# Kernel tuning notes

Measured on AMD Instinct MI355X. Metric: run time of the kernel, lower is better.

The kernel has to match this reference:

```python
import math
import jax, jax.numpy as jnp
import numpy as np

B, T, C, H = 2, 2048, 1024, 16
MAX_SEQ = 2048


def _make_pe(max_seq: int, dim: int, base: float = 10000.0) -> np.ndarray:
    pe = np.zeros((max_seq, dim), dtype=np.float32)
    position = np.arange(max_seq, dtype=np.float32)[:, None]
    div_term = np.exp(np.arange(0, dim, 2, dtype=np.float32) * (-math.log(base) / dim))
    pe[:, 0::2] = np.sin(position * div_term)
    pe[:, 1::2] = np.cos(position * div_term)
    return pe


def setup_inputs() -> dict:
    key = jax.random.key(0)
    k1, k2, k3 = jax.random.split(key, 3)
    x = jax.random.normal(k1, (B, T, C), dtype=jnp.float32)
    # torch Linear default init scale ~ 1/sqrt(fan_in)
    w_qkv = jax.random.normal(k2, (3 * C, C), dtype=jnp.float32) / math.sqrt(C)
    w_proj = jax.random.normal(k3, (C, C), dtype=jnp.float32) / math.sqrt(C)
    pe = jnp.asarray(_make_pe(MAX_SEQ, C))
    return {"x": x, "w_qkv": w_qkv, "w_proj": w_proj, "pe": pe}


def reference(x, w_qkv, w_proj, pe):
    b, t, c = x.shape
    h = H
    d = c // h
    # RoPE module adds sinusoidal PE under torch.no_grad() -> stop_gradient
    xp = jax.lax.stop_gradient(x + pe[None, :t, :])
    qkv = xp @ w_qkv.T  # [b, t, 3c]
    q, k, v = jnp.split(qkv, 3, axis=-1)
    q = q.reshape(b, t, h, d).transpose(0, 2, 1, 3)  # bhtd
    k = k.reshape(b, t, h, d).transpose(0, 2, 1, 3)
    v = v.reshape(b, t, h, d).transpose(0, 2, 1, 3)
    att = jnp.einsum("bhqd,bhkd->bhqk", q, k) * (1.0 / math.sqrt(d))
    causal = jnp.tril(jnp.ones((t, t), dtype=bool))  # [t, t]
    att = jnp.where(causal[None, None], att, -jnp.inf)
    att = jax.nn.softmax(att, axis=-1)
    y = jnp.einsum("bhqk,bhkd->bhqd", att, v)
    y = y.transpose(0, 2, 1, 3).reshape(b, t, c)
    return y @ w_proj.T
```

## Files before the change

kernel.cpp:

```cpp
#include <hip/hip_runtime.h>
#include <cstdint>

typedef __bf16 bf16x8 __attribute__((ext_vector_type(8)));
typedef __bf16 bf16x4 __attribute__((ext_vector_type(4)));
typedef float  f32x4  __attribute__((ext_vector_type(4)));

static constexpr int kB = 2, kT = 2048, kC = 1024, kH = 16, kD = 64;
static constexpr int kK = 1024;

__device__ __forceinline__ uint16_t f2bf(float f) {
  uint32_t u = __builtin_bit_cast(uint32_t, f);
  u += 0x7FFFu + ((u >> 16) & 1u);
  return (uint16_t)(u >> 16);
}

__device__ __forceinline__ void gl_lds16(const void* g, void* l) {
  __builtin_amdgcn_global_load_lds((__attribute__((address_space(1))) void*)(void*)g,
                                   (__attribute__((address_space(3))) void*)l, 16, 0, 0);
}

__global__ __launch_bounds__(256) void prep_all(const float* __restrict__ x,
                                                const float* __restrict__ pe,
                                                const float* __restrict__ wqkv,
                                                const float* __restrict__ wproj,
                                                uint16_t* __restrict__ xp,
                                                uint16_t* __restrict__ wq,
                                                uint16_t* __restrict__ wp) {
  constexpr int NX = kB * kT * kC / 4;
  constexpr int NWQ = 3 * kC * kC / 4;
  const int i = blockIdx.x * 256 + threadIdx.x;
  if (i < NX) {
    const float4 xv = ((const float4*)x)[i];
    const int c4 = i & (kC / 4 - 1);
    const int t = (i / (kC / 4)) & (kT - 1);
    const float4 pv = ((const float4*)pe)[t * (kC / 4) + c4];
    ushort4 o;
    o.x = f2bf(xv.x + pv.x);
    o.y = f2bf(xv.y + pv.y);
    o.z = f2bf(xv.z + pv.z);
    o.w = f2bf(xv.w + pv.w);
    ((ushort4*)xp)[i] = o;
  } else if (i < NX + NWQ) {
    const int j = i - NX;
    const float4 v = ((const float4*)wqkv)[j];
    ushort4 u;
    u.x = f2bf(v.x); u.y = f2bf(v.y); u.z = f2bf(v.z); u.w = f2bf(v.w);
    ((ushort4*)wq)[j] = u;
  } else {
    const int j = i - NX - NWQ;
    const float4 v = ((const float4*)wproj)[j];
    ushort4 u;
    u.x = f2bf(v.x); u.y = f2bf(v.y); u.z = f2bf(v.z); u.w = f2bf(v.w);
    ((ushort4*)wp)[j] = u;
  }
}

__global__ __launch_bounds__(512, 2) void gemm_qkv(const uint16_t* __restrict__ A,
                                                   const uint16_t* __restrict__ W,
                                                   uint16_t* __restrict__ qb,
                                                   uint16_t* __restrict__ kb,
                                                   uint16_t* __restrict__ vT) {
  __shared__ __align__(1024) char lds[114688];
  const int tid = threadIdx.x;
  const int lane = tid & 63;
  const int wid = tid >> 6;
  const int l15 = lane & 15, l4 = lane >> 4;
  const int WM = wid >> 2, WN = wid & 3;
  const int orig = (int)blockIdx.x;
  const int xcd = orig & 7, j = orig >> 3;
  const int m0 = (xcd * 2 + (j & 1)) * 256;
  const int n0 = (j >> 1) * 192;

  f32x4 acc[2][4][3] = {};
  bf16x8 bfp[2][3];

  auto stageA = [&](int buf, int kt) {
#pragma unroll
    for (int c = 0; c < 4; ++c) {
      const int off = (c * 512 + tid) * 16;
      const int lr = off >> 7, cbl = off & 127;
      gl_lds16((const char*)A + ((size_t)(m0 + lr) * kK + kt * 64) * 2 +
                   (cbl ^ ((lr & 7) << 4)),
               lds + buf * 32768 + off);
    }
  };
  auto stageB = [&](int buf, int kt) {
#pragma unroll
    for (int c = 0; c < 3; ++c) {
      const int off = (c * 512 + tid) * 16;
      const int lr = off >> 7, cbl = off & 127;
      gl_lds16((const char*)W + ((size_t)(n0 + lr) * kK + kt * 64) * 2 +
                   (cbl ^ ((lr & 7) << 4)),
               lds + 65536 + buf * 24576 + off);
    }
  };

#define QKV_PHASE(CBUF, H, SA, SBUF, KT, VM)                                      \
  {                                                                               \
    if (SA) stageA(SBUF, KT); else stageB(SBUF, KT);                              \
    if (VM == 4)                                                                  \
      asm volatile("s_waitcnt vmcnt(4)" ::: "memory");                            \
    else                                                                          \
      asm volatile("s_waitcnt vmcnt(7)" ::: "memory");                            \
    __builtin_amdgcn_s_barrier();                                                 \
    asm volatile("" ::: "memory");                                                \
    const char* Ab = lds + (CBUF)*32768;                                          \
    const char* Bb = lds + 65536 + (CBUF)*24576;                                  \
    if ((H) == 0) {                                                               \
      _Pragma("unroll") for (int ks = 0; ks < 2; ++ks)                            \
          _Pragma("unroll") for (int nt = 0; nt < 3; ++nt) {                      \
        const int lr = WN * 48 + nt * 16 + l15;                                   \
        bfp[ks][nt] = *(const bf16x8*)(Bb + lr * 128 +                            \
                                       ((ks * 64 + l4 * 16) ^ ((lr & 7) << 4)));  \
      }                                                                           \
    }                                                                             \
    _Pragma("unroll") for (int ks = 0; ks < 2; ++ks) {                            \
      bf16x8 af[4];                                                               \
      _Pragma("unroll") for (int mt = 0; mt < 4; ++mt) {                          \
        const int lr = (H)*128 + WM * 64 + mt * 16 + l15;                         \
        af[mt] = *(const bf16x8*)(Ab + lr * 128 +                                 \
                                  ((ks * 64 + l4 * 16) ^ ((lr & 7) << 4)));       \
      }                                                                           \
      __builtin_amdgcn_s_setprio(1);                                              \
      _Pragma("unroll") for (int mt = 0; mt < 4; ++mt)                            \
          _Pragma("unroll") for (int nt = 0; nt < 3; ++nt)                        \
              acc[H][mt][nt] = __builtin_amdgcn_mfma_f32_16x16x32_bf16(           \
                  af[mt], bfp[ks][nt], acc[H][mt][nt], 0, 0, 0);                  \
      __builtin_amdgcn_s_setprio(0);                                              \
    }                                                                             \
    asm volatile("" ::: "memory");                                                \
    __builtin_amdgcn_s_barrier();                                                 \
    asm volatile("" ::: "memory");                                                \
  }

  stageA(0, 0);
  stageB(0, 0);

  for (int i = 0; i < 8; ++i) {
    const int ktb1 = 2 * i + 1;
    const int ktb0 = (2 * i + 2 > 15) ? 15 : 2 * i + 2;
    QKV_PHASE(0, 0, 1, 1, ktb1, 4);
    QKV_PHASE(0, 1, 0, 1, ktb1, 7);
    QKV_PHASE(1, 0, 1, 0, ktb0, 4);
    QKV_PHASE(1, 1, 0, 0, ktb0, 7);
  }
  asm volatile("s_waitcnt vmcnt(0)" ::: "memory");
  __builtin_amdgcn_s_barrier();
  asm volatile("" ::: "memory");

  const int b = m0 >> 11, tb = m0 & (kT - 1);
#pragma unroll
  for (int h = 0; h < 2; ++h)
#pragma unroll
    for (int mt = 0; mt < 4; ++mt)
#pragma unroll
      for (int nt = 0; nt < 3; ++nt)
#pragma unroll
        for (int r = 0; r < 4; ++r) {
          const int m = h * 128 + WM * 64 + mt * 16 + l4 * 4 + r;
          const int t = tb + m;
          const int n = n0 + WN * 48 + nt * 16 + l15;
          const int sec = n >> 10, nn = n & (kC - 1);
          const int hh = nn >> 6, d = nn & 63;
          const uint16_t v = f2bf(acc[h][mt][nt][r]);
          if (sec == 0)
            qb[((size_t)((b * kH + hh) * kT + t)) * kD + d] = v;
          else if (sec == 1)
            kb[((size_t)((b * kH + hh) * kT + t)) * kD + d] = v;
          else
            vT[((size_t)((b * kH + hh) * kD + d)) * kT + t] = v;
        }
#undef QKV_PHASE
}

__global__ __launch_bounds__(256, 2) void gemm_proj(const uint16_t* __restrict__ A,
                                                    const uint16_t* __restrict__ W,
                                                    float* __restrict__ out) {
  __shared__ __align__(1024) char lds[65536];
  const int tid = threadIdx.x;
  const int lane = tid & 63;
  const int wid = tid >> 6;
  const int l15 = lane & 15, l4 = lane >> 4;
  const int WM = wid >> 1, WN = wid & 1;
  const int orig = (int)blockIdx.x;
  const int xcd = orig & 7, j = orig >> 3;
  const int m0 = (xcd * 4 + (j & 3)) * 128;
  const int n0 = (j >> 2) * 128;

  f32x4 acc[2][2][4] = {};
  bf16x8 bfp[2][4];

  auto stage = [&](int isA, int buf, int kt) {
#pragma unroll
    for (int c = 0; c < 4; ++c) {
      const int off = (c * 256 + tid) * 16;
      const int lr = off >> 7, cbl = off & 127;
      const size_t grow = (size_t)((isA ? m0 : n0) + lr) * kK + kt * 64;
      gl_lds16((const char*)(isA ? A : W) + grow * 2 + (cbl ^ ((lr & 7) << 4)),
               lds + (isA ? 0 : 32768) + buf * 16384 + off);
    }
  };

#define PRJ_PHASE(CBUF, H, SA, SBUF, KT, VM)                                      \
  {                                                                               \
    stage(SA, SBUF, KT);                                                          \
    if (VM == 4)                                                                  \
      asm volatile("s_waitcnt vmcnt(4)" ::: "memory");                            \
    else                                                                          \
      asm volatile("s_waitcnt vmcnt(8)" ::: "memory");                            \
    __builtin_amdgcn_s_barrier();                                                 \
    asm volatile("" ::: "memory");                                                \
    const char* Ab = lds + (CBUF)*16384;                                          \
    const char* Bb = lds + 32768 + (CBUF)*16384;                                  \
    if ((H) == 0) {                                                               \
      _Pragma("unroll") for (int ks = 0; ks < 2; ++ks)                            \
          _Pragma("unroll") for (int nt = 0; nt < 4; ++nt) {                      \
        const int lr = WN * 64 + nt * 16 + l15;                                   \
        bfp[ks][nt] = *(const bf16x8*)(Bb + lr * 128 +                            \
                                       ((ks * 64 + l4 * 16) ^ ((lr & 7) << 4)));  \
      }                                                                           \
    }                                                                             \
    _Pragma("unroll") for (int ks = 0; ks < 2; ++ks) {                            \
      bf16x8 af[2];                                                               \
      _Pragma("unroll") for (int mt = 0; mt < 2; ++mt) {                          \
        const int lr = (H)*64 + WM * 32 + mt * 16 + l15;                          \
        af[mt] = *(const bf16x8*)(Ab + lr * 128 +                                 \
                                  ((ks * 64 + l4 * 16) ^ ((lr & 7) << 4)));       \
      }                                                                           \
      __builtin_amdgcn_s_setprio(1);                                              \
      _Pragma("unroll") for (int mt = 0; mt < 2; ++mt)                            \
          _Pragma("unroll") for (int nt = 0; nt < 4; ++nt)                        \
              acc[H][mt][nt] = __builtin_amdgcn_mfma_f32_16x16x32_bf16(           \
                  af[mt], bfp[ks][nt], acc[H][mt][nt], 0, 0, 0);                  \
      __builtin_amdgcn_s_setprio(0);                                              \
    }                                                                             \
    asm volatile("" ::: "memory");                                                \
    __builtin_amdgcn_s_barrier();                                                 \
    asm volatile("" ::: "memory");                                                \
  }

  stage(1, 0, 0);
  stage(0, 0, 0);

  for (int i = 0; i < 8; ++i) {
    const int ktb1 = 2 * i + 1;
    const int ktb0 = (2 * i + 2 > 15) ? 15 : 2 * i + 2;
    PRJ_PHASE(0, 0, 1, 1, ktb1, 4);
    PRJ_PHASE(0, 1, 0, 1, ktb1, 8);
    PRJ_PHASE(1, 0, 1, 0, ktb0, 4);
    PRJ_PHASE(1, 1, 0, 0, ktb0, 8);
  }
  asm volatile("s_waitcnt vmcnt(0)" ::: "memory");
  __builtin_amdgcn_s_barrier();
  asm volatile("" ::: "memory");

#pragma unroll
  for (int h = 0; h < 2; ++h)
#pragma unroll
    for (int mt = 0; mt < 2; ++mt)
#pragma unroll
      for (int nt = 0; nt < 4; ++nt)
#pragma unroll
        for (int r = 0; r < 4; ++r) {
          const int m = m0 + h * 64 + WM * 32 + mt * 16 + l4 * 4 + r;
          const int n = n0 + WN * 64 + nt * 16 + l15;
          out[(size_t)m * kC + n] = acc[h][mt][nt][r];
        }
#undef PRJ_PHASE
}

__global__ __launch_bounds__(256, 4) void attn(const uint16_t* __restrict__ qb,
                                               const uint16_t* __restrict__ kb,
                                               const uint16_t* __restrict__ vT,
                                               uint16_t* __restrict__ y) {
  __shared__ __align__(1024) char lds[40960];
  const int lane = threadIdx.x & 63;
  const int wid = threadIdx.x >> 6;
  const int l15 = lane & 15, l4 = lane >> 4;
  const int bh = blockIdx.x;
  const int qt = (int)(gridDim.y - 1) - (int)blockIdx.y;
  const int q0 = qt * 64 + wid * 16;
  const size_t base = (size_t)bh * kT * kD;
  const uint16_t* Q = qb + base;
  const uint16_t* Kp = kb + base;
  const uint16_t* Vt = vT + base;
  char* P = lds + 32768 + wid * 2048;
  const int xr = (l15 & 7) << 4;

  bf16x8 qf[2];
#pragma unroll
  for (int ks = 0; ks < 2; ++ks) {
    bf16x8 t = *(const bf16x8*)(Q + (size_t)(q0 + l15) * kD + ks * 32 + l4 * 8);
#pragma unroll
    for (int i = 0; i < 8; ++i) t[i] = (__bf16)((float)t[i] * 0.1803368801f);
    qf[ks] = t;
  }
  bf16x8 ones;
#pragma unroll
  for (int i = 0; i < 8; ++i) ones[i] = (__bf16)1.0f;

  float m_ = -1e30f;
  f32x4 o[4];
  f32x4 ol = {0.f, 0.f, 0.f, 0.f};
#pragma unroll
  for (int nt = 0; nt < 4; ++nt) o[nt] = (f32x4){0.f, 0.f, 0.f, 0.f};

  const int nkt = qt + 1;

  auto STAGE = [&](int bi, int k0) {
#pragma unroll
    for (int c = 0; c < 2; ++c) {
      const int call = wid * 2 + c;
      const int row = call * 8 + (lane >> 3);
      const int colb = (((lane & 7) ^ ((lane >> 3) & 7)) << 4);
      gl_lds16((const char*)Kp + ((size_t)(k0 + row) * kD) * 2 + colb,
               lds + bi * 8192 + call * 1024);
      gl_lds16((const char*)Vt + ((size_t)row * kT + k0) * 2 + colb,
               lds + 16384 + bi * 8192 + call * 1024);
    }
  };

  int cur = 0;
  STAGE(0, 0);
  for (int kt = 0; kt < nkt; ++kt) {
    const int k0 = kt * 64;
    const bool hasnext = (kt + 1 < nkt);
    if (hasnext) STAGE(cur ^ 1, k0 + 64);
    if (hasnext)
      asm volatile("s_waitcnt vmcnt(4)" ::: "memory");
    else
      asm volatile("s_waitcnt vmcnt(0)" ::: "memory");
    __builtin_amdgcn_s_barrier();
    asm volatile("" ::: "memory");

    const char* Kb = lds + cur * 8192;
    const char* Vb = lds + 16384 + cur * 8192;

    f32x4 s[4] = {};
    __builtin_amdgcn_s_setprio(1);
#pragma unroll
    for (int ks = 0; ks < 2; ++ks)
#pragma unroll
      for (int nt = 0; nt < 4; ++nt) {
        const bf16x8 kf =
            *(const bf16x8*)(Kb + (nt * 16 + l15) * 128 + ((ks * 64 + l4 * 16) ^ xr));
        s[nt] = __builtin_amdgcn_mfma_f32_16x16x32_bf16(kf, qf[ks], s[nt], 0, 0, 0);
      }
    __builtin_amdgcn_s_setprio(0);

    if (kt == nkt - 1) {
      const int qq = q0 + l15;
#pragma unroll
      for (int nt = 0; nt < 4; ++nt)
#pragma unroll
        for (int r = 0; r < 4; ++r)
          if (k0 + nt * 16 + l4 * 4 + r > qq) s[nt][r] = -1e30f;
    }

    float pm = s[0][0];
#pragma unroll
    for (int nt = 0; nt < 4; ++nt)
#pragma unroll
      for (int r = 0; r < 4; ++r) pm = fmaxf(pm, s[nt][r]);
    if (!__all(pm <= m_ + 11.0f)) {
      float rm = fmaxf(pm, __shfl_xor(pm, 16));
      rm = fmaxf(rm, __shfl_xor(rm, 32));
      const float newm = fmaxf(m_, rm);
      const float sc = exp2f(m_ - newm);
      m_ = newm;
#pragma unroll
      for (int nt = 0; nt < 4; ++nt)
#pragma unroll
        for (int r = 0; r < 4; ++r) o[nt][r] *= sc;
#pragma unroll
      for (int r = 0; r < 4; ++r) ol[r] *= sc;
    }
#pragma unroll
    for (int nt = 0; nt < 4; ++nt)
#pragma unroll
      for (int r = 0; r < 4; ++r) s[nt][r] = exp2f(s[nt][r] - m_);

#pragma unroll
    for (int nt = 0; nt < 4; ++nt) {
      bf16x4 pk;
#pragma unroll
      for (int r = 0; r < 4; ++r) pk[r] = (__bf16)s[nt][r];
      *(bf16x4*)(P + l15 * 128 + ((nt * 32 + l4 * 8) ^ xr)) = pk;
    }
    asm volatile("s_waitcnt lgkmcnt(0)" ::: "memory");
    __builtin_amdgcn_sched_barrier(0);

    bf16x8 pf[2];
#pragma unroll
    for (int ks = 0; ks < 2; ++ks)
      pf[ks] = *(const bf16x8*)(P + l15 * 128 + ((ks * 64 + l4 * 16) ^ xr));
    __builtin_amdgcn_s_setprio(1);
#pragma unroll
    for (int ks = 0; ks < 2; ++ks) {
#pragma unroll
      for (int nt = 0; nt < 4; ++nt) {
        const bf16x8 vf =
            *(const bf16x8*)(Vb + (nt * 16 + l15) * 128 + ((ks * 64 + l4 * 16) ^ xr));
        o[nt] = __builtin_amdgcn_mfma_f32_16x16x32_bf16(vf, pf[ks], o[nt], 0, 0, 0);
      }
      ol = __builtin_amdgcn_mfma_f32_16x16x32_bf16(ones, pf[ks], ol, 0, 0, 0);
    }
    __builtin_amdgcn_s_setprio(0);

    __builtin_amdgcn_s_barrier();
    asm volatile("" ::: "memory");
    cur ^= 1;
  }

  const float inv = 1.0f / ol[0];
  const int b = bh >> 4, h = bh & 15;
  const int q = q0 + l15;
#pragma unroll
  for (int nt = 0; nt < 4; ++nt) {
    bf16x4 yv;
#pragma unroll
    for (int r = 0; r < 4; ++r) yv[r] = (__bf16)(o[nt][r] * inv);
    *(bf16x4*)(y + ((size_t)(b * kT + q)) * kC + h * kD + nt * 16 + l4 * 4) = yv;
  }
}

extern "C" void kernel_launch(void* const* d_in, const int* in_sizes, int n_in,
                              void* d_out, int out_size, void* d_ws, size_t ws_size,
                              hipStream_t stream) {
  const float* x = (const float*)d_in[0];
  const float* wqkv = (const float*)d_in[1];
  const float* wproj = (const float*)d_in[2];
  const float* pe = (const float*)d_in[3];

  char* ws = (char*)d_ws;
  uint16_t* xp = (uint16_t*)(ws);
  uint16_t* wq = (uint16_t*)(ws + (size_t)(8u << 20));
  uint16_t* wp = (uint16_t*)(ws + (size_t)(14u << 20));
  uint16_t* qbuf = (uint16_t*)(ws + (size_t)(16u << 20));
  uint16_t* kbuf = (uint16_t*)(ws + (size_t)(24u << 20));
  uint16_t* vTb = (uint16_t*)(ws + (size_t)(32u << 20));

  prep_all<<<dim3(8192), 256, 0, stream>>>(x, pe, wqkv, wproj, xp, wq, wp);

  gemm_qkv<<<dim3(256), 512, 0, stream>>>(xp, wq, qbuf, kbuf, vTb);

  attn<<<dim3(kB * kH, kT / 64), 256, 0, stream>>>(qbuf, kbuf, vTb, xp);

  gemm_proj<<<dim3(256), 256, 0, stream>>>(xp, wp, (float*)d_out);
}
```

Before: 113.9 us.

## Widen QKV GEMM tile, stage V-transpose through LDS, single-barrier attention loop

The QKV GEMM N-tile grows from 192 to 256 columns, so the grid drops from 256 to 192 blocks and each tile lines up with one of the Q/K/V sections. The V-section epilogue now transposes the accumulators through LDS and writes 16-byte coalesced rows into vT, replacing scattered 2-byte strided stores. The attention loop moves the prefetch after one full wait-and-barrier and drops the trailing barrier, trading some load/compute overlap for fewer synchronisations. The larger tile raises LDS use to 128 KB and register pressure, and fewer blocks may leave some CUs idle.

Measured after the change: 100.8 us (median of 2 runs). 11.5% less time.

```diff
diff --git a/kernel.cpp b/kernel.cpp
--- a/kernel.cpp
+++ b/kernel.cpp
@@ -60,7 +60,7 @@
                                                    uint16_t* __restrict__ qb,
                                                    uint16_t* __restrict__ kb,
                                                    uint16_t* __restrict__ vT) {
-  __shared__ __align__(1024) char lds[114688];
+  __shared__ __align__(1024) char lds[131072];
   const int tid = threadIdx.x;
   const int lane = tid & 63;
   const int wid = tid >> 6;
@@ -69,47 +69,37 @@
   const int orig = (int)blockIdx.x;
   const int xcd = orig & 7, j = orig >> 3;
   const int m0 = (xcd * 2 + (j & 1)) * 256;
-  const int n0 = (j >> 1) * 192;
-
-  f32x4 acc[2][4][3] = {};
-  bf16x8 bfp[2][3];
-
-  auto stageA = [&](int buf, int kt) {
+  const int n0 = (j >> 1) * 256;
+
+  f32x4 acc[2][4][4] = {};
+  bf16x8 bfp[2][4];
+
+  auto stage = [&](int isA, int buf, int kt) {
 #pragma unroll
     for (int c = 0; c < 4; ++c) {
       const int off = (c * 512 + tid) * 16;
       const int lr = off >> 7, cbl = off & 127;
-      gl_lds16((const char*)A + ((size_t)(m0 + lr) * kK + kt * 64) * 2 +
-                   (cbl ^ ((lr & 7) << 4)),
-               lds + buf * 32768 + off);
-    }
-  };
-  auto stageB = [&](int buf, int kt) {
-#pragma unroll
-    for (int c = 0; c < 3; ++c) {
-      const int off = (c * 512 + tid) * 16;
-      const int lr = off >> 7, cbl = off & 127;
-      gl_lds16((const char*)W + ((size_t)(n0 + lr) * kK + kt * 64) * 2 +
-                   (cbl ^ ((lr & 7) << 4)),
-               lds + 65536 + buf * 24576 + off);
+      const size_t grow = (size_t)((isA ? m0 : n0) + lr) * kK + kt * 64;
+      gl_lds16((const char*)(isA ? A : W) + grow * 2 + (cbl ^ ((lr & 7) << 4)),
+               lds + (isA ? 0 : 65536) + buf * 32768 + off);
     }
   };
 
 #define QKV_PHASE(CBUF, H, SA, SBUF, KT, VM)                                      \
   {                                                                               \
-    if (SA) stageA(SBUF, KT); else stageB(SBUF, KT);                              \
+    stage(SA, SBUF, KT);                                                          \
     if (VM == 4)                                                                  \
       asm volatile("s_waitcnt vmcnt(4)" ::: "memory");                            \
     else                                                                          \
-      asm volatile("s_waitcnt vmcnt(7)" ::: "memory");                            \
+      asm volatile("s_waitcnt vmcnt(8)" ::: "memory");                            \
     __builtin_amdgcn_s_barrier();                                                 \
     asm volatile("" ::: "memory");                                                \
     const char* Ab = lds + (CBUF)*32768;                                          \
-    const char* Bb = lds + 65536 + (CBUF)*24576;                                  \
+    const char* Bb = lds + 65536 + (CBUF)*32768;                                  \
     if ((H) == 0) {                                                               \
       _Pragma("unroll") for (int ks = 0; ks < 2; ++ks)                            \
-          _Pragma("unroll") for (int nt = 0; nt < 3; ++nt) {                      \
-        const int lr = WN * 48 + nt * 16 + l15;                                   \
+          _Pragma("unroll") for (int nt = 0; nt < 4; ++nt) {                      \
+        const int lr = WN * 64 + nt * 16 + l15;                                   \
         bfp[ks][nt] = *(const bf16x8*)(Bb + lr * 128 +                            \
                                        ((ks * 64 + l4 * 16) ^ ((lr & 7) << 4)));  \
       }                                                                           \
@@ -123,7 +113,7 @@
       }                                                                           \
       __builtin_amdgcn_s_setprio(1);                                              \
       _Pragma("unroll") for (int mt = 0; mt < 4; ++mt)                            \
-          _Pragma("unroll") for (int nt = 0; nt < 3; ++nt)                        \
+          _Pragma("unroll") for (int nt = 0; nt < 4; ++nt)                        \
               acc[H][mt][nt] = __builtin_amdgcn_mfma_f32_16x16x32_bf16(           \
                   af[mt], bfp[ks][nt], acc[H][mt][nt], 0, 0, 0);                  \
       __builtin_amdgcn_s_setprio(0);                                              \
@@ -133,43 +123,68 @@
     asm volatile("" ::: "memory");                                                \
   }
 
-  stageA(0, 0);
-  stageB(0, 0);
+  stage(1, 0, 0);
+  stage(0, 0, 0);
 
   for (int i = 0; i < 8; ++i) {
     const int ktb1 = 2 * i + 1;
     const int ktb0 = (2 * i + 2 > 15) ? 15 : 2 * i + 2;
     QKV_PHASE(0, 0, 1, 1, ktb1, 4);
-    QKV_PHASE(0, 1, 0, 1, ktb1, 7);
+    QKV_PHASE(0, 1, 0, 1, ktb1, 8);
     QKV_PHASE(1, 0, 1, 0, ktb0, 4);
-    QKV_PHASE(1, 1, 0, 0, ktb0, 7);
+    QKV_PHASE(1, 1, 0, 0, ktb0, 8);
   }
   asm volatile("s_waitcnt vmcnt(0)" ::: "memory");
   __builtin_amdgcn_s_barrier();
   asm volatile("" ::: "memory");
 
+  const int sec = n0 >> 10;
   const int b = m0 >> 11, tb = m0 & (kT - 1);
-#pragma unroll
-  for (int h = 0; h < 2; ++h)
-#pragma unroll
-    for (int mt = 0; mt < 4; ++mt)
-#pragma unroll
-      for (int nt = 0; nt < 3; ++nt)
-#pragma unroll
-        for (int r = 0; r < 4; ++r) {
-          const int m = h * 128 + WM * 64 + mt * 16 + l4 * 4 + r;
-          const int t = tb + m;
-          const int n = n0 + WN * 48 + nt * 16 + l15;
-          const int sec = n >> 10, nn = n & (kC - 1);
-          const int hh = nn >> 6, d = nn & 63;
-          const uint16_t v = f2bf(acc[h][mt][nt][r]);
-          if (sec == 0)
-            qb[((size_t)((b * kH + hh) * kT + t)) * kD + d] = v;
-          else if (sec == 1)
-            kb[((size_t)((b * kH + hh) * kT + t)) * kD + d] = v;
-          else
-            vT[((size_t)((b * kH + hh) * kD + d)) * kT + t] = v;
+  if (sec < 2) {
+    uint16_t* dst = (sec == 0) ? qb : kb;
+#pragma unroll
+    for (int h = 0; h < 2; ++h)
+#pragma unroll
+      for (int mt = 0; mt < 4; ++mt)
+#pragma unroll
+        for (int nt = 0; nt < 4; ++nt)
+#pragma unroll
+          for (int r = 0; r < 4; ++r) {
+            const int m = h * 128 + WM * 64 + mt * 16 + l4 * 4 + r;
+            const int nn = (n0 & (kC - 1)) + WN * 64 + nt * 16 + l15;
+            const int hh = nn >> 6, d = nn & 63;
+            dst[((size_t)((b * kH + hh) * kT + tb + m)) * kD + d] =
+                f2bf(acc[h][mt][nt][r]);
+          }
+  } else {
+#pragma unroll
+    for (int h = 0; h < 2; ++h)
+#pragma unroll
+      for (int mt = 0; mt < 4; ++mt)
+#pragma unroll
+        for (int nt = 0; nt < 4; ++nt) {
+          const int nl = WN * 64 + nt * 16 + l15;
+          const int mb2 = (h * 128 + WM * 64 + mt * 16 + l4 * 4) * 2;
+          ushort4 pk;
+          pk.x = f2bf(acc[h][mt][nt][0]);
+          pk.y = f2bf(acc[h][mt][nt][1]);
+          pk.z = f2bf(acc[h][mt][nt][2]);
+          pk.w = f2bf(acc[h][mt][nt][3]);
+          *(ushort4*)(lds + nl * 512 + (mb2 ^ ((nl & 7) << 4))) = pk;
         }
+    asm volatile("" ::: "memory");
+    __builtin_amdgcn_s_barrier();
+    asm volatile("" ::: "memory");
+#pragma unroll
+    for (int it = 0; it < 16; ++it) {
+      const int chunk = it * 512 + tid;
+      const int nr = chunk >> 5, mb = (chunk & 31) * 16;
+      const bf16x8 v = *(const bf16x8*)(lds + nr * 512 + (mb ^ ((nr & 7) << 4)));
+      const int nn = (n0 - 2048) + nr;
+      const int hh = nn >> 6, d = nn & 63;
+      *(bf16x8*)(vT + ((size_t)((b * kH + hh) * kD + d)) * kT + tb + (chunk & 31) * 8) = v;
+    }
+  }
 #undef QKV_PHASE
 }
 
@@ -324,14 +339,10 @@
   STAGE(0, 0);
   for (int kt = 0; kt < nkt; ++kt) {
     const int k0 = kt * 64;
-    const bool hasnext = (kt + 1 < nkt);
-    if (hasnext) STAGE(cur ^ 1, k0 + 64);
-    if (hasnext)
-      asm volatile("s_waitcnt vmcnt(4)" ::: "memory");
-    else
-      asm volatile("s_waitcnt vmcnt(0)" ::: "memory");
+    asm volatile("s_waitcnt vmcnt(0)" ::: "memory");
     __builtin_amdgcn_s_barrier();
     asm volatile("" ::: "memory");
+    if (kt + 1 < nkt) STAGE(cur ^ 1, k0 + 64);
 
     const char* Kb = lds + cur * 8192;
     const char* Vb = lds + 16384 + cur * 8192;
@@ -407,8 +418,6 @@
     }
     __builtin_amdgcn_s_setprio(0);
 
-    __builtin_amdgcn_s_barrier();
-    asm volatile("" ::: "memory");
     cur ^= 1;
   }
 
@@ -442,7 +451,7 @@
 
   prep_all<<<dim3(8192), 256, 0, stream>>>(x, pe, wqkv, wproj, xp, wq, wp);
 
-  gemm_qkv<<<dim3(256), 512, 0, stream>>>(xp, wq, qbuf, kbuf, vTb);
+  gemm_qkv<<<dim3(192), 512, 0, stream>>>(xp, wq, qbuf, kbuf, vTb);
 
   attn<<<dim3(kB * kH, kT / 64), 256, 0, stream>>>(qbuf, kbuf, vTb, xp);
 
```
